# Kernel optimization log

Measured on AMD Instinct MI355X. Metric: run time of the kernel, lower is better.

## Reference

```python
import jax, jax.numpy as jnp
import numpy as np

N_DATA = 40000   # max_training_points
D_PCA = 16       # n_pca_components
D_FEAT = 384     # raw feature dim
Q = 8192         # number of query points


def setup_inputs() -> dict:
    key = jax.random.key(0)
    k1, k2, k3, k4, k5 = jax.random.split(key, 5)
    features = jax.random.normal(k1, (Q, D_FEAT), dtype=jnp.float32)
    pca_mean = jax.random.normal(k2, (D_FEAT,), dtype=jnp.float32) * 0.1
    singular_vectors = jax.random.normal(k3, (D_FEAT, D_PCA), dtype=jnp.float32) / np.sqrt(D_FEAT)
    max_length = jnp.asarray(4.0, dtype=jnp.float32)  # max L2 norm seen at fit time
    # bw_transform is lower-triangular (Cholesky of scaled inverse covariance)
    bw = jax.random.normal(k4, (D_PCA, D_PCA), dtype=jnp.float32) * 0.2
    bw_transform = jnp.tril(bw) + 1.5 * jnp.eye(D_PCA, dtype=jnp.float32)
    dataset = jax.random.normal(k5, (N_DATA, D_PCA), dtype=jnp.float32)  # already bw-transformed at fit
    # norm = prod(diag(bw)) * (2*pi)^(-d/2)
    norm = jnp.prod(jnp.diag(bw_transform)) * jnp.asarray((2 * np.pi) ** (-D_PCA / 2), jnp.float32)
    return {
        'features': features,
        'pca_mean': pca_mean,
        'singular_vectors': singular_vectors,
        'max_length': max_length,
        'bw_transform': bw_transform,
        'dataset': dataset,
        'norm': norm,
    }


def reference(features, pca_mean, singular_vectors, max_length, bw_transform, dataset, norm):
    # PCA.transform: center then project
    f = jnp.matmul(features - pca_mean, singular_vectors)          # [Q, d]
    # pre_process with SCALE method
    f = f / max_length
    # GaussianKDE.forward: bandwidth transform then pairwise sq-dist to dataset
    f = jnp.matmul(f, bw_transform)                                # [Q, d]
    # ||dataset_j - f_i||^2 = |f|^2 + |ds|^2 - 2 f.ds  (vectorized, no QxNxd tensor)
    d2 = (jnp.sum(f * f, axis=1, keepdims=True)
          + jnp.sum(dataset * dataset, axis=1)[None, :]
          - 2.0 * jnp.matmul(f, dataset.T))                        # [Q, N]
    estimate = jnp.mean(jnp.exp(-0.5 * d2), axis=1) * norm         # [Q]
    scores = jnp.log(estimate + 1e-300)                            # log-likelihood
    # compute_probabilities
    return 1.0 / (1.0 + jnp.exp(0.05 * (scores - 12.0)))
```

## Files before the change

### kernel.cpp

```cpp
#include <hip/hip_runtime.h>
#include <hip/hip_bf16.h>

#define Q 8192
#define DF 384
#define DP 16
#define NDATA 40000
#define AUGK 32
#define ROLEA_BLOCKS 128
#define ROLEB_BLOCKS ((NDATA + 255) / 256)
#define NQBLK 64
#define QB_PER_BLK 128

typedef __attribute__((ext_vector_type(8))) short short8v;
typedef __attribute__((ext_vector_type(4))) float f32x4;

__device__ __forceinline__ unsigned short f2bf(float x) {
    union { float f; unsigned int u; } c; c.f = x;
    unsigned int u = c.u;
    u += 0x7fff + ((u >> 16) & 1);
    return (unsigned short)(u >> 16);
}
__device__ __forceinline__ float bf2f(unsigned short h) {
    union { float f; unsigned int u; } c; c.u = ((unsigned int)h) << 16;
    return c.f;
}
__device__ __forceinline__ float fexp2(float x) {
#if __has_builtin(__builtin_amdgcn_exp2f)
    return __builtin_amdgcn_exp2f(x);
#else
    float r; asm volatile("v_exp_f32 %0, %1" : "=v"(r) : "v"(x)); return r;
#endif
}

__global__ __launch_bounds__(256) void k_pre(
    const float* __restrict__ feat, const float* __restrict__ mean,
    const float* __restrict__ sv, const float* __restrict__ bw,
    const float* __restrict__ maxlen_p, const float* __restrict__ ds,
    unsigned short* __restrict__ cfb, float* __restrict__ qb,
    unsigned short* __restrict__ dsb)
{
    int t = threadIdx.x;

    if (blockIdx.x >= ROLEA_BLOCKS) {
        int j = (int)(blockIdx.x - ROLEA_BLOCKS) * 256 + t;
        if (j < NDATA) {
            const float4* r = (const float4*)(ds + (size_t)j * DP);
            unsigned int pk[8];
            float ss = 0.f;
#pragma unroll
            for (int q4 = 0; q4 < 4; ++q4) {
                float4 v = r[q4];
                unsigned short h0 = f2bf(v.x), h1 = f2bf(v.y);
                unsigned short h2 = f2bf(v.z), h3 = f2bf(v.w);
                float f0 = bf2f(h0), f1 = bf2f(h1), f2 = bf2f(h2), f3 = bf2f(h3);
                ss += f0 * f0 + f1 * f1 + f2 * f2 + f3 * f3;
                pk[q4 * 2 + 0] = (unsigned int)h0 | ((unsigned int)h1 << 16);
                pk[q4 * 2 + 1] = (unsigned int)h2 | ((unsigned int)h3 << 16);
            }
            float bj = -0.72134752044f * ss;
            unsigned short hi = f2bf(bj);
            unsigned short lo = f2bf(bj - bf2f(hi));
            uint4* dst = (uint4*)(dsb + (size_t)j * AUGK);
            dst[0] = make_uint4(pk[0], pk[1], pk[2], pk[3]);
            dst[1] = make_uint4(pk[4], pk[5], pk[6], pk[7]);
            dst[2] = make_uint4((unsigned int)hi | ((unsigned int)lo << 16), 0u, 0u, 0u);
            dst[3] = make_uint4(0u, 0u, 0u, 0u);
        }
        return;
    }

    __shared__ float Mlds[DF * DP];
    __shared__ float bwl[256];
    __shared__ float red[256];
    __shared__ float cmp[16];
    __shared__ float cc[16];

    float scale = 1.4426950408889634f / (*maxlen_p);
    bwl[t] = bw[t];
    {
        int k = t & 15, s = t >> 4;
        float a = 0.f;
        for (int d = s; d < DF; d += 16)
            a = fmaf(mean[d], sv[d * DP + k], a);
        red[t] = a;
    }
    __syncthreads();
    if (t < 16) {
        float m = 0.f;
        for (int s = 0; s < 16; ++s) m += red[s * 16 + t];
        cmp[t] = m;
    }
    for (int d = t; d < DF; d += 256) {
        const float4* s4 = (const float4*)(sv + (size_t)d * DP);
        float4 a0 = s4[0], a1 = s4[1], a2 = s4[2], a3 = s4[3];
        float svr[16] = {a0.x, a0.y, a0.z, a0.w, a1.x, a1.y, a1.z, a1.w,
                         a2.x, a2.y, a2.z, a2.w, a3.x, a3.y, a3.z, a3.w};
        float mrow[16];
#pragma unroll
        for (int j = 0; j < 16; ++j) {
            float m = 0.f;
#pragma unroll
            for (int k = 0; k < 16; ++k) m = fmaf(svr[k], bwl[k * 16 + j], m);
            mrow[j] = scale * m;
        }
        float4* md = (float4*)(Mlds + (size_t)d * DP);
        md[0] = make_float4(mrow[0], mrow[1], mrow[2], mrow[3]);
        md[1] = make_float4(mrow[4], mrow[5], mrow[6], mrow[7]);
        md[2] = make_float4(mrow[8], mrow[9], mrow[10], mrow[11]);
        md[3] = make_float4(mrow[12], mrow[13], mrow[14], mrow[15]);
    }
    __syncthreads();
    if (t < 16) {
        float s = 0.f;
#pragma unroll
        for (int k = 0; k < 16; ++k) s = fmaf(cmp[k], bwl[k * 16 + t], s);
        cc[t] = scale * s;
    }
    __syncthreads();

    int row = (int)blockIdx.x * 64 + (t >> 2);
    int dsl = t & 3;
    float acc[16];
#pragma unroll
    for (int k = 0; k < 16; ++k) acc[k] = 0.f;
    const float4* fb = (const float4*)(feat + (size_t)row * DF);
    for (int c = 0; c < DF / 16; ++c) {
        float4 v = fb[c * 4 + dsl];
        int dbase = c * 16 + dsl * 4;
        const float fe[4] = {v.x, v.y, v.z, v.w};
#pragma unroll
        for (int e = 0; e < 4; ++e) {
            const float4* mr = (const float4*)(Mlds + (size_t)(dbase + e) * DP);
            float4 m0 = mr[0], m1 = mr[1], m2 = mr[2], m3 = mr[3];
            acc[0]  = fmaf(fe[e], m0.x, acc[0]);  acc[1]  = fmaf(fe[e], m0.y, acc[1]);
            acc[2]  = fmaf(fe[e], m0.z, acc[2]);  acc[3]  = fmaf(fe[e], m0.w, acc[3]);
            acc[4]  = fmaf(fe[e], m1.x, acc[4]);  acc[5]  = fmaf(fe[e], m1.y, acc[5]);
            acc[6]  = fmaf(fe[e], m1.z, acc[6]);  acc[7]  = fmaf(fe[e], m1.w, acc[7]);
            acc[8]  = fmaf(fe[e], m2.x, acc[8]);  acc[9]  = fmaf(fe[e], m2.y, acc[9]);
            acc[10] = fmaf(fe[e], m2.z, acc[10]); acc[11] = fmaf(fe[e], m2.w, acc[11]);
            acc[12] = fmaf(fe[e], m3.x, acc[12]); acc[13] = fmaf(fe[e], m3.y, acc[13]);
            acc[14] = fmaf(fe[e], m3.z, acc[14]); acc[15] = fmaf(fe[e], m3.w, acc[15]);
        }
    }
#pragma unroll
    for (int k = 0; k < 16; ++k) {
        acc[k] += __shfl_xor(acc[k], 1);
        acc[k] += __shfl_xor(acc[k], 2);
    }
    if (dsl == 0) {
        unsigned int pk[16];
        float s2 = 0.f;
        unsigned short h[16];
#pragma unroll
        for (int k = 0; k < 16; ++k) {
            float f = acc[k] - cc[k];
            h[k] = f2bf(f);
            float fr = bf2f(h[k]);
            s2 += fr * fr;
        }
        qb[row] = -0.34657359028f * s2;
#pragma unroll
        for (int p = 0; p < 8; ++p)
            pk[p] = (unsigned int)h[2 * p] | ((unsigned int)h[2 * p + 1] << 16);
        pk[8] = 0x3F803F80u;
#pragma unroll
        for (int p = 9; p < 16; ++p) pk[p] = 0u;
        uint4* dst = (uint4*)(cfb + (size_t)row * AUGK);
        dst[0] = make_uint4(pk[0], pk[1], pk[2], pk[3]);
        dst[1] = make_uint4(pk[4], pk[5], pk[6], pk[7]);
        dst[2] = make_uint4(pk[8], pk[9], pk[10], pk[11]);
        dst[3] = make_uint4(pk[12], pk[13], pk[14], pk[15]);
    }
}

__global__ __launch_bounds__(256) void k3_main(
    const unsigned short* __restrict__ cfb, const unsigned short* __restrict__ dsb,
    float* __restrict__ partial, int cs)
{
    int qblk = (int)blockIdx.x % NQBLK;
    int c    = (int)blockIdx.x / NQBLK;
    int w = threadIdx.x >> 6, l = threadIdx.x & 63;
    int qbase = qblk * QB_PER_BLK + w * 32;
    int kg = l >> 4, col = l & 15;

    const short8v* ap = (const short8v*)(cfb + (size_t)(qbase + col) * AUGK + kg * 8);
    short8v a0 = ap[0];
    short8v a1 = ap[64];

    int j0 = c * cs;
    int j1 = min(NDATA, j0 + cs);
    int ntile = (j1 - j0) >> 4;

    const short8v* bp = (const short8v*)(dsb + (size_t)(j0 + col) * AUGK + kg * 8);

    float sacc[2][4] = {{0.f, 0.f, 0.f, 0.f}, {0.f, 0.f, 0.f, 0.f}};
    f32x4 z = {0.f, 0.f, 0.f, 0.f};

#pragma unroll 4
    for (int it = 0; it < ntile; ++it) {
        short8v bf = bp[(size_t)it * 64];
        f32x4 d0 = __builtin_amdgcn_mfma_f32_16x16x32_bf16(a0, bf, z, 0, 0, 0);
        f32x4 d1 = __builtin_amdgcn_mfma_f32_16x16x32_bf16(a1, bf, z, 0, 0, 0);
#pragma unroll
        for (int r = 0; r < 4; ++r) {
            sacc[0][r] += fexp2(d0[r]);
            sacc[1][r] += fexp2(d1[r]);
        }
    }

#pragma unroll
    for (int o = 1; o < 16; o <<= 1)
#pragma unroll
        for (int tt = 0; tt < 2; ++tt)
#pragma unroll
            for (int r = 0; r < 4; ++r)
                sacc[tt][r] += __shfl_xor(sacc[tt][r], o);

    if (col == 0) {
        float* dst = partial + (size_t)c * Q + qbase;
#pragma unroll
        for (int tt = 0; tt < 2; ++tt)
#pragma unroll
            for (int r = 0; r < 4; ++r)
                dst[tt * 16 + kg * 4 + r] = sacc[tt][r];
    }
}

__global__ __launch_bounds__(256) void k4_final(
    const float* __restrict__ partial, const float* __restrict__ qb,
    const float* __restrict__ norm_p, float* __restrict__ out, int nd)
{
    __shared__ float l2[8][33];
    int t = threadIdx.x;
    int ql = t & 31, sl = t >> 5;
    int q = (int)blockIdx.x * 32 + ql;
    float a = 0.f;
    for (int cc = sl; cc < nd; cc += 8) a += partial[(size_t)cc * Q + q];
    l2[sl][ql] = a;
    __syncthreads();
    if (t < 32) {
        int qq = (int)blockIdx.x * 32 + t;
        float s = 0.f;
#pragma unroll
        for (int s8 = 0; s8 < 8; ++s8) s += l2[s8][t];
        float est = (*norm_p) * (1.0f / (float)NDATA) * fexp2(qb[qq]) * s;
        float score = logf(est + 1e-38f);
        out[qq] = 1.0f / (1.0f + expf(0.05f * (score - 12.0f)));
    }
}

extern "C" void kernel_launch(void* const* d_in, const int* in_sizes, int n_in,
                              void* d_out, int out_size, void* d_ws, size_t ws_size,
                              hipStream_t stream) {
    const float* features = (const float*)d_in[0];
    const float* pca_mean = (const float*)d_in[1];
    const float* sv       = (const float*)d_in[2];
    const float* maxlen   = (const float*)d_in[3];
    const float* bw       = (const float*)d_in[4];
    const float* dataset  = (const float*)d_in[5];
    const float* norm     = (const float*)d_in[6];
    float* out = (float*)d_out;

    char* ws = (char*)d_ws;
    unsigned short* cfb = (unsigned short*)(ws);
    unsigned short* dsb = (unsigned short*)(ws + 524288);
    float* qb = (float*)(ws + 524288 + 2560000);
    float* partial = (float*)(ws + 524288 + 2560000 + 32768);
    size_t head = 524288 + 2560000 + 32768;

    int nd = 32;
    size_t avail = (ws_size > head) ? (ws_size - head) / ((size_t)Q * 4) : 1;
    if ((size_t)nd > avail) nd = (int)avail;
    if (nd < 1) nd = 1;
    int tiles = NDATA / 16;
    int tpc = (tiles + nd - 1) / nd;
    int cs = tpc * 16;
    nd = (tiles + tpc - 1) / tpc;

    k_pre<<<ROLEA_BLOCKS + ROLEB_BLOCKS, 256, 0, stream>>>(
        features, pca_mean, sv, bw, maxlen, dataset, cfb, qb, dsb);
    k3_main<<<NQBLK * nd, 256, 0, stream>>>(cfb, dsb, partial, cs);
    k4_final<<<Q / 32, 256, 0, stream>>>(partial, qb, norm, out, nd);
}
```

Baseline: 147.2 us.

## Replace exp2 with Schraudolph bit-trick and split precompute into separate kernel

The exponent is pre-scaled by 2^23 with a bias folded into the dataset augmentation column, so the MFMA output converted to int and reinterpreted as float approximates exp2. This replaces the transcendental in the hot loop with a convert plus bit cast. The projection matrix precompute moves into a single-block kernel, and query preprocessing now runs on 512 blocks of 16 rows each instead of 128 blocks that each recomputed the matrix. The exponential is only a piecewise-linear approximation, which may hurt accuracy, and the extra launch adds overhead.

```diff
diff --git a/kernel.cpp b/kernel.cpp
--- a/kernel.cpp
+++ b/kernel.cpp
@@ -6,10 +6,12 @@
 #define DP 16
 #define NDATA 40000
 #define AUGK 32
-#define ROLEA_BLOCKS 128
-#define ROLEB_BLOCKS ((NDATA + 255) / 256)
+#define QPRE_BLOCKS 512
+#define DPRE_BLOCKS ((NDATA + 255) / 256)
 #define NQBLK 64
 #define QB_PER_BLK 128
+#define SCH_C 126.95703125f
+#define P23 8388608.f
 
 typedef __attribute__((ext_vector_type(8))) short short8v;
 typedef __attribute__((ext_vector_type(4))) float f32x4;
@@ -23,6 +25,9 @@
 __device__ __forceinline__ float bf2f(unsigned short h) {
     union { float f; unsigned int u; } c; c.u = ((unsigned int)h) << 16;
     return c.f;
+}
+__device__ __forceinline__ float i2f_bits(int i) {
+    union { int i; float f; } c; c.i = i; return c.f;
 }
 __device__ __forceinline__ float fexp2(float x) {
 #if __has_builtin(__builtin_amdgcn_exp2f)
@@ -32,17 +37,68 @@
 #endif
 }
 
+__global__ __launch_bounds__(384) void k_mm(
+    const float* __restrict__ mean, const float* __restrict__ sv,
+    const float* __restrict__ bw, const float* __restrict__ maxlen_p,
+    float* __restrict__ M2, float* __restrict__ cc)
+{
+    __shared__ float bwl[256];
+    __shared__ float red[384];
+    __shared__ float cmps[16];
+    int t = threadIdx.x;
+    if (t < 256) bwl[t] = bw[t];
+    {
+        int k = t & 15, s = t >> 4;
+        float a = 0.f;
+        for (int d = s; d < DF; d += 24)
+            a = fmaf(mean[d], sv[d * DP + k], a);
+        red[t] = a;
+    }
+    __syncthreads();
+    float scale = P23 * 1.4426950408889634f / (*maxlen_p);
+    {
+        const float4* s4 = (const float4*)(sv + (size_t)t * DP);
+        float4 a0 = s4[0], a1 = s4[1], a2 = s4[2], a3 = s4[3];
+        float svr[16] = {a0.x, a0.y, a0.z, a0.w, a1.x, a1.y, a1.z, a1.w,
+                         a2.x, a2.y, a2.z, a2.w, a3.x, a3.y, a3.z, a3.w};
+        float mrow[16];
+#pragma unroll
+        for (int j = 0; j < 16; ++j) {
+            float m = 0.f;
+#pragma unroll
+            for (int k = 0; k < 16; ++k) m = fmaf(svr[k], bwl[k * 16 + j], m);
+            mrow[j] = scale * m;
+        }
+        float4* md = (float4*)(M2 + (size_t)t * DP);
+        md[0] = make_float4(mrow[0], mrow[1], mrow[2], mrow[3]);
+        md[1] = make_float4(mrow[4], mrow[5], mrow[6], mrow[7]);
+        md[2] = make_float4(mrow[8], mrow[9], mrow[10], mrow[11]);
+        md[3] = make_float4(mrow[12], mrow[13], mrow[14], mrow[15]);
+    }
+    if (t < 16) {
+        float m = 0.f;
+        for (int s = 0; s < 24; ++s) m += red[s * 16 + t];
+        cmps[t] = m;
+    }
+    __syncthreads();
+    if (t < 16) {
+        float s = 0.f;
+#pragma unroll
+        for (int k = 0; k < 16; ++k) s = fmaf(cmps[k], bwl[k * 16 + t], s);
+        cc[t] = scale * s;
+    }
+}
+
 __global__ __launch_bounds__(256) void k_pre(
-    const float* __restrict__ feat, const float* __restrict__ mean,
-    const float* __restrict__ sv, const float* __restrict__ bw,
-    const float* __restrict__ maxlen_p, const float* __restrict__ ds,
+    const float* __restrict__ feat, const float* __restrict__ ds,
+    const float* __restrict__ M2, const float* __restrict__ cc,
     unsigned short* __restrict__ cfb, float* __restrict__ qb,
     unsigned short* __restrict__ dsb)
 {
     int t = threadIdx.x;
 
-    if (blockIdx.x >= ROLEA_BLOCKS) {
-        int j = (int)(blockIdx.x - ROLEA_BLOCKS) * 256 + t;
+    if (blockIdx.x >= QPRE_BLOCKS) {
+        int j = (int)(blockIdx.x - QPRE_BLOCKS) * 256 + t;
         if (j < NDATA) {
             const float4* r = (const float4*)(ds + (size_t)j * DP);
             unsigned int pk[8];
@@ -57,9 +113,9 @@
                 pk[q4 * 2 + 0] = (unsigned int)h0 | ((unsigned int)h1 << 16);
                 pk[q4 * 2 + 1] = (unsigned int)h2 | ((unsigned int)h3 << 16);
             }
-            float bj = -0.72134752044f * ss;
-            unsigned short hi = f2bf(bj);
-            unsigned short lo = f2bf(bj - bf2f(hi));
+            float v = fmaf(ss, -0.72134752044f, SCH_C);
+            unsigned short hi = f2bf(v);
+            unsigned short lo = f2bf(v - bf2f(hi));
             uint4* dst = (uint4*)(dsb + (size_t)j * AUGK);
             dst[0] = make_uint4(pk[0], pk[1], pk[2], pk[3]);
             dst[1] = make_uint4(pk[4], pk[5], pk[6], pk[7]);
@@ -69,100 +125,62 @@
         return;
     }
 
-    __shared__ float Mlds[DF * DP];
-    __shared__ float bwl[256];
-    __shared__ float red[256];
-    __shared__ float cmp[16];
-    __shared__ float cc[16];
-
-    float scale = 1.4426950408889634f / (*maxlen_p);
-    bwl[t] = bw[t];
-    {
-        int k = t & 15, s = t >> 4;
-        float a = 0.f;
-        for (int d = s; d < DF; d += 16)
-            a = fmaf(mean[d], sv[d * DP + k], a);
-        red[t] = a;
-    }
+    __shared__ __align__(16) float m2l[DF * 20];
+    __shared__ float ccl[16];
+    const float4* m2g = (const float4*)M2;
+#pragma unroll
+    for (int it = 0; it < 6; ++it) {
+        int i = it * 256 + t;
+        int d = i >> 2, qq = i & 3;
+        *(float4*)(m2l + d * 20 + qq * 4) = m2g[i];
+    }
+    if (t < 16) ccl[t] = cc[t];
     __syncthreads();
-    if (t < 16) {
-        float m = 0.f;
-        for (int s = 0; s < 16; ++s) m += red[s * 16 + t];
-        cmp[t] = m;
-    }
-    for (int d = t; d < DF; d += 256) {
-        const float4* s4 = (const float4*)(sv + (size_t)d * DP);
-        float4 a0 = s4[0], a1 = s4[1], a2 = s4[2], a3 = s4[3];
-        float svr[16] = {a0.x, a0.y, a0.z, a0.w, a1.x, a1.y, a1.z, a1.w,
-                         a2.x, a2.y, a2.z, a2.w, a3.x, a3.y, a3.z, a3.w};
-        float mrow[16];
-#pragma unroll
-        for (int j = 0; j < 16; ++j) {
-            float m = 0.f;
-#pragma unroll
-            for (int k = 0; k < 16; ++k) m = fmaf(svr[k], bwl[k * 16 + j], m);
-            mrow[j] = scale * m;
-        }
-        float4* md = (float4*)(Mlds + (size_t)d * DP);
-        md[0] = make_float4(mrow[0], mrow[1], mrow[2], mrow[3]);
-        md[1] = make_float4(mrow[4], mrow[5], mrow[6], mrow[7]);
-        md[2] = make_float4(mrow[8], mrow[9], mrow[10], mrow[11]);
-        md[3] = make_float4(mrow[12], mrow[13], mrow[14], mrow[15]);
-    }
-    __syncthreads();
-    if (t < 16) {
-        float s = 0.f;
-#pragma unroll
-        for (int k = 0; k < 16; ++k) s = fmaf(cmp[k], bwl[k * 16 + t], s);
-        cc[t] = scale * s;
-    }
-    __syncthreads();
-
-    int row = (int)blockIdx.x * 64 + (t >> 2);
-    int dsl = t & 3;
+
+    int r = t >> 4, s = t & 15;
+    int row = (int)blockIdx.x * 16 + r;
     float acc[16];
 #pragma unroll
     for (int k = 0; k < 16; ++k) acc[k] = 0.f;
-    const float4* fb = (const float4*)(feat + (size_t)row * DF);
-    for (int c = 0; c < DF / 16; ++c) {
-        float4 v = fb[c * 4 + dsl];
-        int dbase = c * 16 + dsl * 4;
-        const float fe[4] = {v.x, v.y, v.z, v.w};
-#pragma unroll
-        for (int e = 0; e < 4; ++e) {
-            const float4* mr = (const float4*)(Mlds + (size_t)(dbase + e) * DP);
-            float4 m0 = mr[0], m1 = mr[1], m2 = mr[2], m3 = mr[3];
-            acc[0]  = fmaf(fe[e], m0.x, acc[0]);  acc[1]  = fmaf(fe[e], m0.y, acc[1]);
-            acc[2]  = fmaf(fe[e], m0.z, acc[2]);  acc[3]  = fmaf(fe[e], m0.w, acc[3]);
-            acc[4]  = fmaf(fe[e], m1.x, acc[4]);  acc[5]  = fmaf(fe[e], m1.y, acc[5]);
-            acc[6]  = fmaf(fe[e], m1.z, acc[6]);  acc[7]  = fmaf(fe[e], m1.w, acc[7]);
-            acc[8]  = fmaf(fe[e], m2.x, acc[8]);  acc[9]  = fmaf(fe[e], m2.y, acc[9]);
-            acc[10] = fmaf(fe[e], m2.z, acc[10]); acc[11] = fmaf(fe[e], m2.w, acc[11]);
-            acc[12] = fmaf(fe[e], m3.x, acc[12]); acc[13] = fmaf(fe[e], m3.y, acc[13]);
-            acc[14] = fmaf(fe[e], m3.z, acc[14]); acc[15] = fmaf(fe[e], m3.w, acc[15]);
-        }
+    const float* fr = feat + (size_t)row * DF;
+#pragma unroll 4
+    for (int c = 0; c < 24; ++c) {
+        int d = s + (c << 4);
+        float fv = fr[d];
+        const float4* mr = (const float4*)(m2l + d * 20);
+        float4 m0 = mr[0], m1 = mr[1], m2 = mr[2], m3 = mr[3];
+        acc[0]  = fmaf(fv, m0.x, acc[0]);  acc[1]  = fmaf(fv, m0.y, acc[1]);
+        acc[2]  = fmaf(fv, m0.z, acc[2]);  acc[3]  = fmaf(fv, m0.w, acc[3]);
+        acc[4]  = fmaf(fv, m1.x, acc[4]);  acc[5]  = fmaf(fv, m1.y, acc[5]);
+        acc[6]  = fmaf(fv, m1.z, acc[6]);  acc[7]  = fmaf(fv, m1.w, acc[7]);
+        acc[8]  = fmaf(fv, m2.x, acc[8]);  acc[9]  = fmaf(fv, m2.y, acc[9]);
+        acc[10] = fmaf(fv, m2.z, acc[10]); acc[11] = fmaf(fv, m2.w, acc[11]);
+        acc[12] = fmaf(fv, m3.x, acc[12]); acc[13] = fmaf(fv, m3.y, acc[13]);
+        acc[14] = fmaf(fv, m3.z, acc[14]); acc[15] = fmaf(fv, m3.w, acc[15]);
     }
 #pragma unroll
     for (int k = 0; k < 16; ++k) {
         acc[k] += __shfl_xor(acc[k], 1);
         acc[k] += __shfl_xor(acc[k], 2);
-    }
-    if (dsl == 0) {
+        acc[k] += __shfl_xor(acc[k], 4);
+        acc[k] += __shfl_xor(acc[k], 8);
+    }
+    if (s == 0) {
         unsigned int pk[16];
+        unsigned short h[16];
         float s2 = 0.f;
-        unsigned short h[16];
 #pragma unroll
         for (int k = 0; k < 16; ++k) {
-            float f = acc[k] - cc[k];
+            float f = acc[k] - ccl[k];
             h[k] = f2bf(f);
-            float fr = bf2f(h[k]);
-            s2 += fr * fr;
+            float fr2 = bf2f(h[k]) * (1.f / P23);
+            s2 += fr2 * fr2;
         }
         qb[row] = -0.34657359028f * s2;
 #pragma unroll
         for (int p = 0; p < 8; ++p)
             pk[p] = (unsigned int)h[2 * p] | ((unsigned int)h[2 * p + 1] << 16);
-        pk[8] = 0x3F803F80u;
+        pk[8] = 0x4B004B00u;
 #pragma unroll
         for (int p = 9; p < 16; ++p) pk[p] = 0u;
         uint4* dst = (uint4*)(cfb + (size_t)row * AUGK);
@@ -203,8 +221,8 @@
         f32x4 d1 = __builtin_amdgcn_mfma_f32_16x16x32_bf16(a1, bf, z, 0, 0, 0);
 #pragma unroll
         for (int r = 0; r < 4; ++r) {
-            sacc[0][r] += fexp2(d0[r]);
-            sacc[1][r] += fexp2(d1[r]);
+            sacc[0][r] += i2f_bits((int)d0[r]);
+            sacc[1][r] += i2f_bits((int)d1[r]);
         }
     }
 
@@ -265,8 +283,10 @@
     unsigned short* cfb = (unsigned short*)(ws);
     unsigned short* dsb = (unsigned short*)(ws + 524288);
     float* qb = (float*)(ws + 524288 + 2560000);
-    float* partial = (float*)(ws + 524288 + 2560000 + 32768);
-    size_t head = 524288 + 2560000 + 32768;
+    float* M2 = (float*)(ws + 524288 + 2560000 + 32768);
+    float* cc = (float*)(ws + 524288 + 2560000 + 32768 + 24576);
+    float* partial = (float*)(ws + 524288 + 2560000 + 32768 + 24576 + 256);
+    size_t head = 524288 + 2560000 + 32768 + 24576 + 256;
 
     int nd = 32;
     size_t avail = (ws_size > head) ? (ws_size - head) / ((size_t)Q * 4) : 1;
@@ -277,8 +297,9 @@
     int cs = tpc * 16;
     nd = (tiles + tpc - 1) / tpc;
 
-    k_pre<<<ROLEA_BLOCKS + ROLEB_BLOCKS, 256, 0, stream>>>(
-        features, pca_mean, sv, bw, maxlen, dataset, cfb, qb, dsb);
+    k_mm<<<1, 384, 0, stream>>>(pca_mean, sv, bw, maxlen, M2, cc);
+    k_pre<<<QPRE_BLOCKS + DPRE_BLOCKS, 256, 0, stream>>>(
+        features, dataset, M2, cc, cfb, qb, dsb);
     k3_main<<<NQBLK * nd, 256, 0, stream>>>(cfb, dsb, partial, cs);
     k4_final<<<Q / 32, 256, 0, stream>>>(partial, qb, norm, out, nd);
 }
```

After: 128.0 us. 1.15x faster.
